# Kernel tuning notes

Hardware: AMD Instinct MI355X
Metric: run time of the kernel (lower is better)

## Reference

```python
import jax, jax.numpy as jnp
import numpy as np

NUM_BINS = 32
SIGMA_RATIO = 0.5          # Gaussian Parzen window width relative to bin spacing
SMOOTH_NR = 1e-07
SMOOTH_DR = 1e-07


def setup_inputs() -> dict:
    key = jax.random.key(0)
    k1, k2 = jax.random.split(key)
    shape = (2, 1, 96, 96, 96)
    pred = jax.random.uniform(k1, shape, dtype=jnp.float32)
    target = jax.random.uniform(k2, shape, dtype=jnp.float32)
    return {"pred": pred, "target": target}


def _parzen_weights(img_flat, bin_centers, preterm):
    # img_flat: [B, N]; bin_centers: [nb]
    # Gaussian Parzen window, normalized so each voxel's weights sum to 1 over bins.
    d = img_flat[..., None] - bin_centers          # [B, N, nb]
    w = jnp.exp(-preterm * d * d)                  # [B, N, nb]
    return w / jnp.sum(w, axis=-1, keepdims=True)


def reference(pred, target):
    B = pred.shape[0]
    nb = NUM_BINS
    bin_centers = jnp.linspace(0.0, 1.0, nb, dtype=jnp.float32)  # [nb]
    bin_width = 1.0 / (nb - 1)
    sigma = SIGMA_RATIO * bin_width
    preterm = jnp.float32(1.0 / (2.0 * sigma * sigma))

    p = pred.reshape(B, -1)    # [B, N]
    t = target.reshape(B, -1)  # [B, N]
    N = p.shape[1]

    wa = _parzen_weights(p, bin_centers, preterm)  # [B, N, nb]
    wb = _parzen_weights(t, bin_centers, preterm)  # [B, N, nb]

    # joint histogram [B, nb, nb] and marginals [B, 1, nb]
    pab = jnp.einsum('bni,bnj->bij', wa, wb) / N
    pa = jnp.mean(wa, axis=1, keepdims=True).transpose(0, 2, 1).transpose(0, 2, 1)  # [B,1,nb]
    pa = jnp.mean(wa, axis=1)[:, None, :]  # [B, 1, nb]
    pb = jnp.mean(wb, axis=1)[:, None, :]  # [B, 1, nb]

    # papb = bmm(pa^T, pb): outer product of marginals -> [B, nb, nb]
    papb = jnp.einsum('bki,bkj->bij', pa, pb)

    mi = jnp.sum(pab * jnp.log((pab + SMOOTH_NR) / (papb + SMOOTH_DR) + SMOOTH_DR),
                 axis=(-1, -2))  # [B]
    return -jnp.mean(mi)
```

## Files before the change

### kernel.cpp

```cpp
#include <hip/hip_runtime.h>
#include <hip/hip_bf16.h>

#define NBINS 32
#define CHUNK 128
#define STR 136
#define TILE_HALVES (NBINS * STR)
#define NTHREADS 256
#define NVOX 884736
#define BPB 512
#define NSLOTS 8

typedef __attribute__((ext_vector_type(8))) _Float16 half8;
typedef __attribute__((ext_vector_type(16))) float f32x16;
typedef __attribute__((ext_vector_type(4))) int i32x4;

__device__ __forceinline__ void compute_w(float x, int& kb, _Float16* wq) {
    float tt = x * 31.0f;
    float kf = rintf(tt);
    int ki = (int)kf;
    float u = tt - kf;
    kb = ki - 3 + (u > 0.0f ? 1 : 0);
    float w[6];
    float s = 0.0f;
#pragma unroll
    for (int o = 0; o < 6; ++o) {
        int b = kb + o;
        float d = tt - (float)b;
        float e = __expf(-2.0f * d * d);
        bool valid = (b >= 0) && (b < NBINS);
        e = valid ? e : 0.0f;
        w[o] = e;
        s += e;
    }
    float rinv = 1.0f / s;
#pragma unroll
    for (int o = 0; o < 6; ++o) wq[o] = (_Float16)(w[o] * rinv);
}

__device__ __forceinline__ void scatter(_Float16* __restrict__ L, int col, int kb_new,
                                        const _Float16* wq, int kb_old, bool zero_old) {
    if (zero_old) {
#pragma unroll
        for (int o = 0; o < 6; ++o) {
            int b = kb_old + o;
            if (b >= 0 && b < NBINS) L[b * STR + col] = (_Float16)0.0f;
        }
    }
#pragma unroll
    for (int o = 0; o < 6; ++o) {
        int b = kb_new + o;
        if (b >= 0 && b < NBINS) L[b * STR + col] = wq[o];
    }
}

__global__ __launch_bounds__(NTHREADS, 4)
void mi_hist_kernel(const float* __restrict__ pred, const float* __restrict__ targ,
                    float* __restrict__ hist ) {
    __shared__ __attribute__((aligned(16))) _Float16 smem[4 * TILE_HALVES];

    const int tid = threadIdx.x;
    const int bx = blockIdx.x;
    const int batch = blockIdx.y;
    const int col = tid & 127;
    const bool isB = tid >= 128;
    const float* src = (isB ? targ : pred) + (size_t)batch * NVOX;
    const int tile_off = isB ? TILE_HALVES : 0;

    const int wid = tid >> 6;
    const int lane = tid & 63;
    const int frag = (lane & 31) * STR + wid * 32 + 8 * (lane >> 5);

    const int nchunks = (bx < 256) ? 14 : 13;

    f32x16 acc;
#pragma unroll
    for (int r = 0; r < 16; ++r) acc[r] = 0.0f;

    {
        i32x4 z = {0, 0, 0, 0};
        i32x4* zp = (i32x4*)smem;
        for (int i = tid; i < (4 * TILE_HALVES) / 8; i += NTHREADS) zp[i] = z;
    }
    float x = src[(size_t)bx * CHUNK + col];
    int kb_old[2] = {0, 0};
    __syncthreads();

#pragma unroll 1
    for (int c = 0; c < nchunks; ++c) {
        const int q = c & 1;
        _Float16 wq[6];
        int kb;
        compute_w(x, kb, wq);
        if (c + 1 < nchunks) {
            x = src[((size_t)(c + 1) * BPB + bx) * CHUNK + col];
        }
        __syncthreads();
        scatter(smem + q * 2 * TILE_HALVES + tile_off, col, kb, wq, kb_old[q], c >= 2);
        kb_old[q] = kb;
        if (c >= 1) {
            const _Float16* Pp = smem + (q ^ 1) * 2 * TILE_HALVES;
#pragma unroll
            for (int kk = 0; kk < 2; ++kk) {
                half8 af = *(const half8*)&Pp[frag + kk * 16];
                half8 bf = *(const half8*)&Pp[TILE_HALVES + frag + kk * 16];
                acc = __builtin_amdgcn_mfma_f32_32x32x16_f16(af, bf, acc, 0, 0, 0);
            }
        }
    }
    __syncthreads();
    {
        const int q = (nchunks - 1) & 1;
        const _Float16* Pp = smem + q * 2 * TILE_HALVES;
#pragma unroll
        for (int kk = 0; kk < 2; ++kk) {
            half8 af = *(const half8*)&Pp[frag + kk * 16];
            half8 bf = *(const half8*)&Pp[TILE_HALVES + frag + kk * 16];
            acc = __builtin_amdgcn_mfma_f32_32x32x16_f16(af, bf, acc, 0, 0, 0);
        }
    }
    __syncthreads();

    float* red = (float*)smem;
    const int colc = lane & 31;
    const int rlo = 4 * (lane >> 5);
#pragma unroll
    for (int r = 0; r < 16; ++r) {
        int rowc = (r & 3) + 8 * (r >> 2) + rlo;
        red[wid * 1024 + rowc * 32 + colc] = acc[r];
    }
    __syncthreads();
    float* H = hist + ((size_t)(bx & (NSLOTS - 1)) * 2 + batch) * 1024;
    for (int idx = tid; idx < 1024; idx += NTHREADS) {
        float s = red[idx] + red[1024 + idx] + red[2048 + idx] + red[3072 + idx];
        atomicAdd(&H[idx], s);
    }
}

__global__ void mi_reduce_kernel(const float* __restrict__ hist, float* __restrict__ out) {
    __shared__ float s_pab[2 * NBINS * NBINS];
    __shared__ double s_pa[2][NBINS];
    __shared__ double s_pb[2][NBINS];
    __shared__ double s_red[256];
    const int tid = threadIdx.x;
    const double invN = 1.0 / (double)NVOX;

    for (int g = tid; g < 512; g += 256) {
        float4 s = make_float4(0.f, 0.f, 0.f, 0.f);
        for (int sl = 0; sl < NSLOTS; ++sl) {
            float4 v = ((const float4*)hist)[sl * 512 + g];
            s.x += v.x; s.y += v.y; s.z += v.z; s.w += v.w;
        }
        ((float4*)s_pab)[g] = s;
    }
    __syncthreads();

    if (tid < 64) {
        int b = tid >> 5, i = tid & 31;
        double s = 0.0;
        for (int j = 0; j < NBINS; ++j) s += (double)s_pab[(b * NBINS + i) * NBINS + j];
        s_pa[b][i] = s * invN;
    } else if (tid < 128) {
        int t2 = tid - 64;
        int b = t2 >> 5, j = t2 & 31;
        double s = 0.0;
        for (int i = 0; i < NBINS; ++i) s += (double)s_pab[(b * NBINS + i) * NBINS + j];
        s_pb[b][j] = s * invN;
    }
    __syncthreads();

    double acc = 0.0;
    for (int idx = tid; idx < 2 * NBINS * NBINS; idx += 256) {
        int b = idx >> 10;
        int cell = idx & 1023;
        int i = cell >> 5, j = cell & 31;
        double pab = (double)s_pab[idx] * invN;
        double papb = s_pa[b][i] * s_pb[b][j];
        acc += pab * log((pab + 1e-7) / (papb + 1e-7) + 1e-7);
    }
    s_red[tid] = acc;
    __syncthreads();
    for (int s2 = 128; s2 > 0; s2 >>= 1) {
        if (tid < s2) s_red[tid] += s_red[tid + s2];
        __syncthreads();
    }
    if (tid == 0) out[0] = (float)(-0.5 * s_red[0]);
}

extern "C" void kernel_launch(void* const* d_in, const int* in_sizes, int n_in,
                              void* d_out, int out_size, void* d_ws, size_t ws_size,
                              hipStream_t stream) {
    const float* pred = (const float*)d_in[0];
    const float* targ = (const float*)d_in[1];
    float* hist = (float*)d_ws;
    float* out = (float*)d_out;

    hipMemsetAsync(hist, 0, NSLOTS * 2 * NBINS * NBINS * sizeof(float), stream);
    dim3 grid(BPB, 2);
    hipLaunchKernelGGL(mi_hist_kernel, grid, dim3(NTHREADS), 0, stream, pred, targ, hist);
    hipLaunchKernelGGL(mi_reduce_kernel, dim3(1), dim3(256), 0, stream, hist, out);
}
```

Measured before the change: 33.48 us.

## Prefetch all chunk inputs upfront, fully unroll chunk loop, use padded branchless scatter rows

All 13-14 per-thread input values are loaded into registers at kernel start instead of one-ahead prefetching, exposing all global loads at once. The chunk loop is fully unrolled with a peeled tail for the extra chunk. The LDS tiles gain two padding rows so scatter and zero writes clamp out-of-range bins into dummy rows instead of branching. This raises register pressure and LDS footprint, which could reduce occupancy.

```diff
diff --git a/kernel.cpp b/kernel.cpp
--- a/kernel.cpp
+++ b/kernel.cpp
@@ -3,8 +3,9 @@
 
 #define NBINS 32
 #define CHUNK 128
+#define NROWS 34
 #define STR 136
-#define TILE_HALVES (NBINS * STR)
+#define TILE_HALVES (NROWS * STR)
 #define NTHREADS 256
 #define NVOX 884736
 #define BPB 512
@@ -27,8 +28,7 @@
         int b = kb + o;
         float d = tt - (float)b;
         float e = __expf(-2.0f * d * d);
-        bool valid = (b >= 0) && (b < NBINS);
-        e = valid ? e : 0.0f;
+        e = ((unsigned)b < NBINS) ? e : 0.0f;
         w[o] = e;
         s += e;
     }
@@ -37,19 +37,19 @@
     for (int o = 0; o < 6; ++o) wq[o] = (_Float16)(w[o] * rinv);
 }
 
-__device__ __forceinline__ void scatter(_Float16* __restrict__ L, int col, int kb_new,
-                                        const _Float16* wq, int kb_old, bool zero_old) {
-    if (zero_old) {
-#pragma unroll
-        for (int o = 0; o < 6; ++o) {
-            int b = kb_old + o;
-            if (b >= 0 && b < NBINS) L[b * STR + col] = (_Float16)0.0f;
-        }
-    }
+__device__ __forceinline__ void zero6(_Float16* __restrict__ L, int col, int kb) {
 #pragma unroll
     for (int o = 0; o < 6; ++o) {
-        int b = kb_new + o;
-        if (b >= 0 && b < NBINS) L[b * STR + col] = wq[o];
+        int r = min(max(kb + o, -1), 32) + 1;
+        L[r * STR + col] = (_Float16)0.0f;
+    }
+}
+__device__ __forceinline__ void scatter6(_Float16* __restrict__ L, int col, int kb,
+                                         const _Float16* wq) {
+#pragma unroll
+    for (int o = 0; o < 6; ++o) {
+        int r = min(max(kb + o, -1), 32) + 1;
+        L[r * STR + col] = wq[o];
     }
 }
 
@@ -64,59 +64,70 @@
     const int col = tid & 127;
     const bool isB = tid >= 128;
     const float* src = (isB ? targ : pred) + (size_t)batch * NVOX;
-    const int tile_off = isB ? TILE_HALVES : 0;
+    const int toff = isB ? TILE_HALVES : 0;
 
     const int wid = tid >> 6;
     const int lane = tid & 63;
-    const int frag = (lane & 31) * STR + wid * 32 + 8 * (lane >> 5);
-
-    const int nchunks = (bx < 256) ? 14 : 13;
-
-    f32x16 acc;
-#pragma unroll
-    for (int r = 0; r < 16; ++r) acc[r] = 0.0f;
+    const int frag = (1 + (lane & 31)) * STR + wid * 32 + 8 * (lane >> 5);
+
+    float xs[14];
+#pragma unroll
+    for (int c = 0; c < 13; ++c)
+        xs[c] = src[((size_t)(c * BPB + bx)) * CHUNK + col];
+    const bool extra = (bx < 256);
+    if (extra) xs[13] = src[((size_t)(13 * BPB + bx)) * CHUNK + col];
 
     {
         i32x4 z = {0, 0, 0, 0};
         i32x4* zp = (i32x4*)smem;
-        for (int i = tid; i < (4 * TILE_HALVES) / 8; i += NTHREADS) zp[i] = z;
-    }
-    float x = src[(size_t)bx * CHUNK + col];
-    int kb_old[2] = {0, 0};
-    __syncthreads();
-
-#pragma unroll 1
-    for (int c = 0; c < nchunks; ++c) {
-        const int q = c & 1;
+#pragma unroll
+        for (int i = 0; i < 10; ++i) {
+            int idx = i * NTHREADS + tid;
+            if (idx < (4 * TILE_HALVES) / 8) zp[idx] = z;
+        }
+    }
+
+    f32x16 acc;
+#pragma unroll
+    for (int r = 0; r < 16; ++r) acc[r] = 0.0f;
+
+    int kbo0 = 0, kbo1 = 0;
+
+#define DO_MFMA(BASE) { \
+        const _Float16* Pp = (BASE); \
+        _Pragma("unroll") \
+        for (int kk = 0; kk < 2; ++kk) { \
+            half8 af = *(const half8*)&Pp[frag + kk * 16]; \
+            half8 bf = *(const half8*)&Pp[TILE_HALVES + frag + kk * 16]; \
+            acc = __builtin_amdgcn_mfma_f32_32x32x16_f16(af, bf, acc, 0, 0, 0); \
+        } }
+
+#pragma unroll
+    for (int c = 0; c < 13; ++c) {
         _Float16 wq[6];
         int kb;
-        compute_w(x, kb, wq);
-        if (c + 1 < nchunks) {
-            x = src[((size_t)(c + 1) * BPB + bx) * CHUNK + col];
-        }
-        __syncthreads();
-        scatter(smem + q * 2 * TILE_HALVES + tile_off, col, kb, wq, kb_old[q], c >= 2);
-        kb_old[q] = kb;
-        if (c >= 1) {
-            const _Float16* Pp = smem + (q ^ 1) * 2 * TILE_HALVES;
-#pragma unroll
-            for (int kk = 0; kk < 2; ++kk) {
-                half8 af = *(const half8*)&Pp[frag + kk * 16];
-                half8 bf = *(const half8*)&Pp[TILE_HALVES + frag + kk * 16];
-                acc = __builtin_amdgcn_mfma_f32_32x32x16_f16(af, bf, acc, 0, 0, 0);
-            }
-        }
-    }
-    __syncthreads();
-    {
-        const int q = (nchunks - 1) & 1;
-        const _Float16* Pp = smem + q * 2 * TILE_HALVES;
-#pragma unroll
-        for (int kk = 0; kk < 2; ++kk) {
-            half8 af = *(const half8*)&Pp[frag + kk * 16];
-            half8 bf = *(const half8*)&Pp[TILE_HALVES + frag + kk * 16];
-            acc = __builtin_amdgcn_mfma_f32_32x32x16_f16(af, bf, acc, 0, 0, 0);
-        }
+        compute_w(xs[c], kb, wq);
+        __syncthreads();
+        _Float16* cur = smem + (c & 1) * 2 * TILE_HALVES + toff;
+        if (c >= 2) zero6(cur, col, (c & 1) ? kbo1 : kbo0);
+        scatter6(cur, col, kb, wq);
+        if (c & 1) kbo1 = kb; else kbo0 = kb;
+        if (c >= 1) DO_MFMA(smem + (((c & 1) ^ 1) * 2) * TILE_HALVES);
+    }
+    if (extra) {
+        _Float16 wq[6];
+        int kb;
+        compute_w(xs[13], kb, wq);
+        __syncthreads();
+        _Float16* cur = smem + 2 * TILE_HALVES + toff;
+        zero6(cur, col, kbo1);
+        scatter6(cur, col, kb, wq);
+        DO_MFMA(smem);
+        __syncthreads();
+        DO_MFMA(smem + 2 * TILE_HALVES);
+    } else {
+        __syncthreads();
+        DO_MFMA(smem);
     }
     __syncthreads();
 
```

New measurement: 31.05 us. 7.3% less time.
